# Kernel optimization log

Measured on AMD Instinct MI355X. Metric: run time of the kernel, lower is better.

Reference implementation:

```python
import jax, jax.numpy as jnp
import numpy as np

B, N, K, C = 8, 4096, 32, 64
RADIUS = 0.15
CIN = C + 3  # dp_fj: concat(dp[3], fj[C])


def _ball_query(p, radius, k):
    """p: (B,N,3). Returns neighbor indices (B,N,K): first k points (in index
    order) within radius of each query, padded with the first valid neighbor
    (ballquery semantics; query point itself is always index 0 candidate)."""
    sq = jnp.sum(p * p, axis=-1)                                  # (B,N)
    d2 = sq[:, :, None] + sq[:, None, :] - 2.0 * jnp.einsum('bnd,bmd->bnm', p, p)
    n = p.shape[1]
    within = d2 <= radius * radius
    key = jnp.where(within, jnp.arange(n, dtype=jnp.int32)[None, None, :], n)
    order = jnp.argsort(key, axis=-1)[..., :k]                    # (B,N,K)
    valid = jnp.take_along_axis(key, order, axis=-1) < n
    first = order[..., :1]
    return jnp.where(valid, order, first)


def _conv2d_1x1(x, w, b):
    # x: (B,Cin,N,K), w: (Cout,Cin), b: (Cout,)
    return jnp.einsum('oi,bink->bonk', w, x) + b[None, :, None, None]


def _conv1d_1x1(x, w, b):
    # x: (B,Cin,N)
    return jnp.einsum('oi,bin->bon', w, x) + b[None, :, None]


def setup_inputs() -> dict:
    key = jax.random.key(0)
    ks = jax.random.split(key, 16)
    s = 0.05
    inp = {
        'p': jax.random.uniform(ks[0], (B, N, 3), dtype=jnp.float32),
        'f': jax.random.normal(ks[1], (B, C, N), dtype=jnp.float32),
        # attn_local: convblock2d (CIN -> C), no act
        'w_attn': jax.random.normal(ks[2], (C, CIN), dtype=jnp.float32) * s,
        'b_attn': jnp.zeros((C,), jnp.float32),
        # convs: convblock2d (CIN -> C, relu) then (C -> C, no act)
        'w1': jax.random.normal(ks[3], (C, CIN), dtype=jnp.float32) * s,
        'b1': jnp.zeros((C,), jnp.float32),
        'w2': jax.random.normal(ks[4], (C, C), dtype=jnp.float32) * s,
        'b2': jnp.zeros((C,), jnp.float32),
        # ffn: convblock1d (C -> C*expansion=C, relu) then (C -> C, no act)
        'wf1': jax.random.normal(ks[5], (C, C), dtype=jnp.float32) * s,
        'bf1': jnp.zeros((C,), jnp.float32),
        'wf2': jax.random.normal(ks[6], (C, C), dtype=jnp.float32) * s,
        'bf2': jnp.zeros((C,), jnp.float32),
    }
    return inp


def reference(p, f, w_attn, b_attn, w1, b1, w2, b2, wf1, bf1, wf2, bf2):
    bidx = jnp.arange(B)[:, None, None]
    idx = _ball_query(p, RADIUS, K)                               # (B,N,K) int
    pj = p[bidx, idx]                                             # (B,N,K,3)
    dp = (pj - p[:, :, None, :]).transpose(0, 3, 1, 2)            # (B,3,N,K)
    ft = f.transpose(0, 2, 1)                                     # (B,N,C)
    fj = ft[bidx, idx].transpose(0, 3, 1, 2)                      # (B,C,N,K)

    fj_cat = jnp.concatenate([dp, fj], axis=1)                    # (B,CIN,N,K)

    attn = _conv2d_1x1(fj_cat, w_attn, b_attn)                    # (B,C,N,K)
    x = jax.nn.relu(_conv2d_1x1(fj_cat, w1, b1))
    x = _conv2d_1x1(x, w2, b2)                                    # (B,C,N,K)

    # new_attention, 4D path: softmax over neighbor axis (tau=1), weighted sum
    channel_attn = jax.nn.softmax(attn, axis=-1)
    fout = jnp.sum(channel_attn * x, axis=-1)                     # (B,C,N)

    fout = jax.nn.relu(fout + f)
    identity = fout
    h = jax.nn.relu(_conv1d_1x1(fout, wf1, bf1))
    h = _conv1d_1x1(h, wf2, bf2)
    fout = jax.nn.relu(h + identity)                              # use_res
    return (p, fout)
```

## Files before the change

kernel.cpp:

```cpp
#include <hip/hip_runtime.h>

#define B_ 8
#define N_ 4096
#define K_ 32
#define C_ 64
#define CIN_ 67
#define R2_ 0.0225f

#define SFJ 104
#define SY1 72
#define SFB 72
#define PTS 4
#define ITERS 4

typedef short short8v __attribute__((ext_vector_type(8)));
typedef short short4v __attribute__((ext_vector_type(4)));
typedef float floatx4 __attribute__((ext_vector_type(4)));

__device__ __forceinline__ short f2bf(float x) {
    return (short)__builtin_bit_cast(unsigned short, (__bf16)x);
}

template <int CTRL>
__device__ __forceinline__ float dpp_add(float x) {
    const int m = __builtin_amdgcn_update_dpp(0, __float_as_int(x), CTRL, 0xF, 0xF, false);
    return x + __int_as_float(m);
}
__device__ __forceinline__ float row16_sum(float x) {
    x = dpp_add<0xB1>(x);
    x = dpp_add<0x4E>(x);
    x = dpp_add<0x141>(x);
    x = dpp_add<0x140>(x);
    return x;
}

__global__ __launch_bounds__(256) void prep_kernel(
    const float* __restrict__ p, const float* __restrict__ f,
    unsigned short* __restrict__ ftb, float4* __restrict__ p4,
    float* __restrict__ pout)
{
#pragma clang fp contract(off)
    __shared__ short tile[64 * 72];
    const int t = threadIdx.x;
    const int b = blockIdx.x >> 6;
    const int n0 = (blockIdx.x & 63) * 64;
    const int nn4 = t & 15, ch = t >> 4;
    for (int cc = 0; cc < 4; ++cc) {
        const int c = cc * 16 + ch;
        const float4 v = *(const float4*)&f[((size_t)(b * 64 + c)) * N_ + n0 + nn4 * 4];
        tile[(nn4 * 4 + 0) * 72 + c] = f2bf(v.x);
        tile[(nn4 * 4 + 1) * 72 + c] = f2bf(v.y);
        tile[(nn4 * 4 + 2) * 72 + c] = f2bf(v.z);
        tile[(nn4 * 4 + 3) * 72 + c] = f2bf(v.w);
    }
    if (t < 48) {
        const size_t base = ((size_t)(b * N_ + n0)) * 3;
        ((float4*)(pout + base))[t] = ((const float4*)(p + base))[t];
    }
    if (t < 64) {
        const int n = n0 + t;
        const float x = p[((size_t)(b * N_ + n)) * 3 + 0];
        const float y = p[((size_t)(b * N_ + n)) * 3 + 1];
        const float z = p[((size_t)(b * N_ + n)) * 3 + 2];
        const float sq = (x * x + y * y) + z * z;
        p4[(size_t)b * N_ + n] = make_float4(x, y, z, sq);
    }
    __syncthreads();
    const int nn = t >> 2, cb = (t & 3) * 16;
    uint4* dst = (uint4*)&ftb[((size_t)(b * N_ + n0 + nn)) * 64 + cb];
    const uint4* src = (const uint4*)&tile[nn * 72 + cb];
    dst[0] = src[0];
    dst[1] = src[1];
}

__global__ __launch_bounds__(256) void ball_query_kernel(
    const float4* __restrict__ p4, unsigned short* __restrict__ idx)
{
#pragma clang fp contract(off)
    const int lane = threadIdx.x & 63;
    const int wid = (blockIdx.x * blockDim.x + threadIdx.x) >> 6;
    const int q0 = wid * 4;
    const int b = q0 >> 12;
    const float4* pb = p4 + (size_t)b * N_;

    float4 Q[4];
    #pragma unroll
    for (int q = 0; q < 4; ++q)
        Q[q] = pb[(q0 + q) & (N_ - 1)];
    int count[4] = {0, 0, 0, 0};
    int first[4] = {-1, -1, -1, -1};
    for (int base = 0; base < N_; base += 64) {
        const float4 A = pb[base + lane];
        unsigned long long m[4];
        bool w[4];
        #pragma unroll
        for (int q = 0; q < 4; ++q) {
            const float d2 = (Q[q].w + A.w)
                - 2.0f * ((Q[q].x * A.x + Q[q].y * A.y) + Q[q].z * A.z);
            w[q] = (d2 <= R2_);
            m[q] = __ballot(w[q]);
        }
        const unsigned long long below = (1ull << lane) - 1ull;
        #pragma unroll
        for (int q = 0; q < 4; ++q) {
            if (m[q]) {
                if (first[q] < 0) first[q] = base + __builtin_ctzll(m[q]);
                if (w[q]) {
                    const int pos = count[q] + __popcll(m[q] & below);
                    if (pos < K_)
                        idx[(size_t)(q0 + q) * K_ + pos] = (unsigned short)(base + lane);
                }
                count[q] += __popcll(m[q]);
            }
        }
        if (count[0] >= K_ && count[1] >= K_ && count[2] >= K_ && count[3] >= K_)
            break;
    }
    #pragma unroll
    for (int q = 0; q < 4; ++q)
        for (int pos = count[q] + lane; pos < K_; pos += 64)
            idx[(size_t)(q0 + q) * K_ + pos] = (unsigned short)first[q];
}

__global__ __launch_bounds__(256) void lpa_mfma_kernel(
    const float4* __restrict__ p4, const float* __restrict__ f,
    const unsigned short* __restrict__ ftb,
    const float* __restrict__ w_attn, const float* __restrict__ b_attn,
    const float* __restrict__ w1, const float* __restrict__ b1,
    const float* __restrict__ w2, const float* __restrict__ b2,
    const float* __restrict__ wf1, const float* __restrict__ bf1,
    const float* __restrict__ wf2, const float* __restrict__ bf2,
    const unsigned short* __restrict__ idx, float* __restrict__ out)
{
    __shared__ __align__(16) short s_fj[128 * SFJ];
    __shared__ __align__(16) short s_y1[128 * SY1];
    __shared__ __align__(16) short s_fbuf[2 * 16 * SFB];
    __shared__ float s_vec[PTS * ITERS * 64];
    short* s_vecbf = s_fbuf;
    short* s_hbf   = s_fbuf + 16 * SFB;

    const int t = threadIdx.x;
    const int lane = t & 63;
    const int mb = t >> 6;
    const int l15 = lane & 15;
    const int quad = lane >> 4;

    short8v wa_f[3], w1_f[3], w2_f[2], wf1_f[2], wf2_f[2];
    {
        const int cm = mb * 16 + l15;
        #pragma unroll
        for (int ks = 0; ks < 3; ++ks) {
            short8v a, bq;
            #pragma unroll
            for (int j = 0; j < 8; ++j) {
                const int ip = ks * 32 + quad * 8 + j;
                float va = 0.0f, vb = 0.0f;
                if (ip < 64)      { va = w_attn[cm * CIN_ + ip + 3];  vb = w1[cm * CIN_ + ip + 3]; }
                else if (ip < 67) { va = w_attn[cm * CIN_ + ip - 64]; vb = w1[cm * CIN_ + ip - 64]; }
                a[j] = f2bf(va); bq[j] = f2bf(vb);
            }
            wa_f[ks] = a; w1_f[ks] = bq;
        }
        #pragma unroll
        for (int ks = 0; ks < 2; ++ks) {
            short8v a, bq, cq;
            #pragma unroll
            for (int j = 0; j < 8; ++j) {
                const int kk = ks * 32 + quad * 8 + j;
                a[j]  = f2bf(w2[cm * 64 + kk]);
                bq[j] = f2bf(wf1[cm * 64 + kk]);
                cq[j] = f2bf(wf2[cm * 64 + kk]);
            }
            w2_f[ks] = a; wf1_f[ks] = bq; wf2_f[ks] = cq;
        }
    }

    const int crow = mb * 16 + quad * 4;
    const float4 bav  = *(const float4*)&b_attn[crow];
    const float4 b1v  = *(const float4*)&b1[crow];
    const float4 b2v  = *(const float4*)&b2[crow];
    const float4 bf1v = *(const float4*)&bf1[crow];
    const float4 bf2v = *(const float4*)&bf2[crow];

    for (int e = t; e < 512; e += 256) {
        const int col = e >> 2, c4 = e & 3;
        *(uint4*)&s_fj[col * SFJ + 72 + c4 * 8] = make_uint4(0u, 0u, 0u, 0u);
    }
    for (int e = t; e < 1152; e += 256) ((unsigned*)s_fbuf)[e] = 0u;

    const int pt00 = blockIdx.x * (PTS * ITERS);
    const int bb = pt00 >> 12;
    const float4* pb = p4 + (size_t)bb * N_;

    const int col = t >> 1, h = t & 1;

    {
        const int j = idx[(size_t)pt00 * K_ + col];
        const uint4* src = (const uint4*)&ftb[((size_t)(bb * N_ + j)) * 64 + h * 32];
        uint4* dst = (uint4*)&s_fj[col * SFJ + h * 32];
        dst[0] = src[0]; dst[1] = src[1]; dst[2] = src[2]; dst[3] = src[3];
        if (h) {
            const int n = (pt00 + (col >> 5)) & (N_ - 1);
            const float4 Pj = pb[j];
            const float4 Pn = pb[n];
            short8v dp = {};
            dp[0] = f2bf(Pj.x - Pn.x);
            dp[1] = f2bf(Pj.y - Pn.y);
            dp[2] = f2bf(Pj.z - Pn.z);
            *(short8v*)&s_fj[col * SFJ + 64] = dp;
        }
    }
    __syncthreads();

    for (int itn = 0; itn < ITERS; ++itn) {
        const int pt0 = pt00 + itn * PTS;

        const bool pf = (itn + 1 < ITERS);
        uint4 g0, g1, g2, g3;
        float4 Pjn, Pnn;
        if (pf) {
            const int jn = idx[(size_t)(pt0 + PTS) * K_ + col];
            const uint4* src = (const uint4*)&ftb[((size_t)(bb * N_ + jn)) * 64 + h * 32];
            g0 = src[0]; g1 = src[1]; g2 = src[2]; g3 = src[3];
            Pjn = pb[jn];
            Pnn = pb[(pt0 + PTS + (col >> 5)) & (N_ - 1)];
        }

        floatx4 accA[8];
        #pragma unroll
        for (int nt = 0; nt < 8; ++nt) {
            const short* bp = &s_fj[(nt * 16 + l15) * SFJ + quad * 8];
            const short8v fb0 = *(const short8v*)(bp);
            const short8v fb1 = *(const short8v*)(bp + 32);
            const short8v fb2 = *(const short8v*)(bp + 64);
            floatx4 a = {0.f, 0.f, 0.f, 0.f};
            a = __builtin_amdgcn_mfma_f32_16x16x32_bf16(wa_f[0], fb0, a, 0, 0, 0);
            a = __builtin_amdgcn_mfma_f32_16x16x32_bf16(wa_f[1], fb1, a, 0, 0, 0);
            a = __builtin_amdgcn_mfma_f32_16x16x32_bf16(wa_f[2], fb2, a, 0, 0, 0);
            accA[nt] = a;
            floatx4 y = {0.f, 0.f, 0.f, 0.f};
            y = __builtin_amdgcn_mfma_f32_16x16x32_bf16(w1_f[0], fb0, y, 0, 0, 0);
            y = __builtin_amdgcn_mfma_f32_16x16x32_bf16(w1_f[1], fb1, y, 0, 0, 0);
            y = __builtin_amdgcn_mfma_f32_16x16x32_bf16(w1_f[2], fb2, y, 0, 0, 0);
            short4v yp;
            yp[0] = f2bf(fmaxf(y[0] + b1v.x, 0.f));
            yp[1] = f2bf(fmaxf(y[1] + b1v.y, 0.f));
            yp[2] = f2bf(fmaxf(y[2] + b1v.z, 0.f));
            yp[3] = f2bf(fmaxf(y[3] + b1v.w, 0.f));
            *(short4v*)&s_y1[(nt * 16 + l15) * SY1 + crow] = yp;
        }
        __syncthreads();

        if (pf) {
            uint4* dst = (uint4*)&s_fj[col * SFJ + h * 32];
            dst[0] = g0; dst[1] = g1; dst[2] = g2; dst[3] = g3;
            if (h) {
                short8v dp = {};
                dp[0] = f2bf(Pjn.x - Pnn.x);
                dp[1] = f2bf(Pjn.y - Pnn.y);
                dp[2] = f2bf(Pjn.z - Pnn.z);
                *(short8v*)&s_fj[col * SFJ + 64] = dp;
            }
        }

        const int nb0 = pt0 & (N_ - 1);
        float4 f4r[4];
        #pragma unroll
        for (int r = 0; r < 4; ++r)
            f4r[r] = *(const float4*)&f[((size_t)(bb * 64 + crow + r)) * N_ + nb0];

        #pragma unroll
        for (int pi = 0; pi < PTS; ++pi) {
            floatx4 xx0, xx1;
            {
                const short* bp = &s_y1[((2 * pi) * 16 + l15) * SY1 + quad * 8];
                const short8v yb0 = *(const short8v*)(bp);
                const short8v yb1 = *(const short8v*)(bp + 32);
                floatx4 x = {0.f, 0.f, 0.f, 0.f};
                x = __builtin_amdgcn_mfma_f32_16x16x32_bf16(w2_f[0], yb0, x, 0, 0, 0);
                x = __builtin_amdgcn_mfma_f32_16x16x32_bf16(w2_f[1], yb1, x, 0, 0, 0);
                xx0 = x;
            }
            {
                const short* bp = &s_y1[((2 * pi + 1) * 16 + l15) * SY1 + quad * 8];
                const short8v yb0 = *(const short8v*)(bp);
                const short8v yb1 = *(const short8v*)(bp + 32);
                floatx4 x = {0.f, 0.f, 0.f, 0.f};
                x = __builtin_amdgcn_mfma_f32_16x16x32_bf16(w2_f[0], yb0, x, 0, 0, 0);
                x = __builtin_amdgcn_mfma_f32_16x16x32_bf16(w2_f[1], yb1, x, 0, 0, 0);
                xx1 = x;
            }
            float fo[4];
            #pragma unroll
            for (int r = 0; r < 4; ++r) {
                const float ba = (r == 0) ? bav.x : (r == 1) ? bav.y : (r == 2) ? bav.z : bav.w;
                const float bx = (r == 0) ? b2v.x : (r == 1) ? b2v.y : (r == 2) ? b2v.z : b2v.w;
                const float e0 = __expf(accA[2 * pi][r] + ba);
                const float e1 = __expf(accA[2 * pi + 1][r] + ba);
                const float t01 = e0 + e1;
                const float se = row16_sum(t01);
                const float sw = row16_sum(e0 * xx0[r] + e1 * xx1[r] + t01 * bx);
                const float fres = (pi == 0) ? f4r[r].x : (pi == 1) ? f4r[r].y
                                 : (pi == 2) ? f4r[r].z : f4r[r].w;
                fo[r] = fmaxf(sw * __builtin_amdgcn_rcpf(se) + fres, 0.f);
            }
            if (l15 == 0) {
                const int prow = itn * PTS + pi;
                *(float4*)&s_vec[prow * 64 + crow] = make_float4(fo[0], fo[1], fo[2], fo[3]);
                short4v fb;
                fb[0] = f2bf(fo[0]); fb[1] = f2bf(fo[1]);
                fb[2] = f2bf(fo[2]); fb[3] = f2bf(fo[3]);
                *(short4v*)&s_vecbf[prow * SFB + crow] = fb;
            }
        }
        __syncthreads();
    }

    {
        const short8v vb0 = *(const short8v*)&s_vecbf[l15 * SFB + quad * 8];
        const short8v vb1 = *(const short8v*)&s_vecbf[l15 * SFB + 32 + quad * 8];
        floatx4 d = {0.f, 0.f, 0.f, 0.f};
        d = __builtin_amdgcn_mfma_f32_16x16x32_bf16(wf1_f[0], vb0, d, 0, 0, 0);
        d = __builtin_amdgcn_mfma_f32_16x16x32_bf16(wf1_f[1], vb1, d, 0, 0, 0);
        short4v hb;
        hb[0] = f2bf(fmaxf(d[0] + bf1v.x, 0.f));
        hb[1] = f2bf(fmaxf(d[1] + bf1v.y, 0.f));
        hb[2] = f2bf(fmaxf(d[2] + bf1v.z, 0.f));
        hb[3] = f2bf(fmaxf(d[3] + bf1v.w, 0.f));
        *(short4v*)&s_hbf[l15 * SFB + crow] = hb;
    }
    __syncthreads();

    {
        const short8v hb0 = *(const short8v*)&s_hbf[l15 * SFB + quad * 8];
        const short8v hb1 = *(const short8v*)&s_hbf[l15 * SFB + 32 + quad * 8];
        floatx4 d = {0.f, 0.f, 0.f, 0.f};
        d = __builtin_amdgcn_mfma_f32_16x16x32_bf16(wf2_f[0], hb0, d, 0, 0, 0);
        d = __builtin_amdgcn_mfma_f32_16x16x32_bf16(wf2_f[1], hb1, d, 0, 0, 0);
        const int n = (pt00 + l15) & (N_ - 1);
        out[((size_t)(bb * 64 + crow + 0)) * N_ + n] =
            fmaxf(d[0] + bf2v.x + s_vec[l15 * 64 + crow + 0], 0.f);
        out[((size_t)(bb * 64 + crow + 1)) * N_ + n] =
            fmaxf(d[1] + bf2v.y + s_vec[l15 * 64 + crow + 1], 0.f);
        out[((size_t)(bb * 64 + crow + 2)) * N_ + n] =
            fmaxf(d[2] + bf2v.z + s_vec[l15 * 64 + crow + 2], 0.f);
        out[((size_t)(bb * 64 + crow + 3)) * N_ + n] =
            fmaxf(d[3] + bf2v.w + s_vec[l15 * 64 + crow + 3], 0.f);
    }
}

extern "C" void kernel_launch(void* const* d_in, const int* in_sizes, int n_in,
                              void* d_out, int out_size, void* d_ws, size_t ws_size,
                              hipStream_t stream)
{
    const float* p      = (const float*)d_in[0];
    const float* f      = (const float*)d_in[1];
    const float* w_attn = (const float*)d_in[2];
    const float* b_attn = (const float*)d_in[3];
    const float* w1     = (const float*)d_in[4];
    const float* b1     = (const float*)d_in[5];
    const float* w2     = (const float*)d_in[6];
    const float* b2     = (const float*)d_in[7];
    const float* wf1    = (const float*)d_in[8];
    const float* bf1    = (const float*)d_in[9];
    const float* wf2    = (const float*)d_in[10];
    const float* bf2    = (const float*)d_in[11];
    float* out = (float*)d_out;

    unsigned short* idx = (unsigned short*)d_ws;
    unsigned short* ftb = (unsigned short*)((char*)d_ws + 2u * 1024 * 1024);
    float4* p4          = (float4*)((char*)d_ws + 6u * 1024 * 1024);

    prep_kernel<<<B_ * (N_ / 64), 256, 0, stream>>>(p, f, ftb, p4, out);
    ball_query_kernel<<<(B_ * N_) / 16, 256, 0, stream>>>(p4, idx);
    lpa_mfma_kernel<<<(B_ * N_) / (PTS * ITERS), 256, 0, stream>>>(
        p4, f, ftb, w_attn, b_attn, w1, b1, w2, b2, wf1, bf1, wf2, bf2,
        idx, out + (size_t)B_ * N_ * 3);
}
```

Before: 222.2 us.

## Double-buffer LDS tiles with XOR swizzle and drop a per-iteration barrier

Replaces padded LDS rows with an unpadded 64-column layout using an XOR swizzle to avoid bank conflicts. The dp channels move to a separate small buffer, injected only by quad 0 for the third k-slice. The fj and y1 tiles are double-buffered so one barrier per iteration replaces two. This cuts barrier stalls and LDS footprint, at the cost of extra index math and a more delicate ordering between writing the next buffer and reading the current one.

```diff
diff --git a/kernel.cpp b/kernel.cpp
--- a/kernel.cpp
+++ b/kernel.cpp
@@ -7,9 +7,6 @@
 #define CIN_ 67
 #define R2_ 0.0225f
 
-#define SFJ 104
-#define SY1 72
-#define SFB 72
 #define PTS 4
 #define ITERS 4
 
@@ -132,12 +129,13 @@
     const float* __restrict__ wf2, const float* __restrict__ bf2,
     const unsigned short* __restrict__ idx, float* __restrict__ out)
 {
-    __shared__ __align__(16) short s_fj[128 * SFJ];
-    __shared__ __align__(16) short s_y1[128 * SY1];
-    __shared__ __align__(16) short s_fbuf[2 * 16 * SFB];
-    __shared__ float s_vec[PTS * ITERS * 64];
+    __shared__ __align__(16) short s_fj[2][128 * 64];
+    __shared__ __align__(16) short s_dp[2][128 * 8];
+    __shared__ __align__(16) short s_y1[2][128 * 64];
+    __shared__ __align__(16) short s_fbuf[2 * 16 * 64];
+    __shared__ float s_vec[16 * 64];
     short* s_vecbf = s_fbuf;
-    short* s_hbf   = s_fbuf + 16 * SFB;
+    short* s_hbf   = s_fbuf + 16 * 64;
 
     const int t = threadIdx.x;
     const int lane = t & 63;
@@ -182,23 +180,21 @@
     const float4 bf1v = *(const float4*)&bf1[crow];
     const float4 bf2v = *(const float4*)&bf2[crow];
 
-    for (int e = t; e < 512; e += 256) {
-        const int col = e >> 2, c4 = e & 3;
-        *(uint4*)&s_fj[col * SFJ + 72 + c4 * 8] = make_uint4(0u, 0u, 0u, 0u);
-    }
-    for (int e = t; e < 1152; e += 256) ((unsigned*)s_fbuf)[e] = 0u;
-
     const int pt00 = blockIdx.x * (PTS * ITERS);
     const int bb = pt00 >> 12;
     const float4* pb = p4 + (size_t)bb * N_;
 
     const int col = t >> 1, h = t & 1;
+    const int gsw = (col & 7) << 3;
 
     {
         const int j = idx[(size_t)pt00 * K_ + col];
         const uint4* src = (const uint4*)&ftb[((size_t)(bb * N_ + j)) * 64 + h * 32];
-        uint4* dst = (uint4*)&s_fj[col * SFJ + h * 32];
-        dst[0] = src[0]; dst[1] = src[1]; dst[2] = src[2]; dst[3] = src[3];
+        const int rb = col * 64;
+        *(uint4*)&s_fj[0][rb + ((h * 32 + 0)  ^ gsw)] = src[0];
+        *(uint4*)&s_fj[0][rb + ((h * 32 + 8)  ^ gsw)] = src[1];
+        *(uint4*)&s_fj[0][rb + ((h * 32 + 16) ^ gsw)] = src[2];
+        *(uint4*)&s_fj[0][rb + ((h * 32 + 24) ^ gsw)] = src[3];
         if (h) {
             const int n = (pt00 + (col >> 5)) & (N_ - 1);
             const float4 Pj = pb[j];
@@ -207,13 +203,14 @@
             dp[0] = f2bf(Pj.x - Pn.x);
             dp[1] = f2bf(Pj.y - Pn.y);
             dp[2] = f2bf(Pj.z - Pn.z);
-            *(short8v*)&s_fj[col * SFJ + 64] = dp;
+            *(short8v*)&s_dp[0][col * 8] = dp;
         }
     }
     __syncthreads();
 
     for (int itn = 0; itn < ITERS; ++itn) {
         const int pt0 = pt00 + itn * PTS;
+        const int cur = itn & 1, nxt = cur ^ 1;
 
         const bool pf = (itn + 1 < ITERS);
         uint4 g0, g1, g2, g3;
@@ -229,10 +226,14 @@
         floatx4 accA[8];
         #pragma unroll
         for (int nt = 0; nt < 8; ++nt) {
-            const short* bp = &s_fj[(nt * 16 + l15) * SFJ + quad * 8];
-            const short8v fb0 = *(const short8v*)(bp);
-            const short8v fb1 = *(const short8v*)(bp + 32);
-            const short8v fb2 = *(const short8v*)(bp + 64);
+            const int row = nt * 16 + l15;
+            const int sw = (l15 & 7) << 3;
+            const short* bp = &s_fj[cur][row * 64];
+            const short8v fb0 = *(const short8v*)(bp + ((quad * 8) ^ sw));
+            const short8v fb1 = *(const short8v*)(bp + ((32 + quad * 8) ^ sw));
+            const short8v dpv = *(const short8v*)&s_dp[cur][row * 8];
+            short8v fb2 = {};
+            if (quad == 0) fb2 = dpv;
             floatx4 a = {0.f, 0.f, 0.f, 0.f};
             a = __builtin_amdgcn_mfma_f32_16x16x32_bf16(wa_f[0], fb0, a, 0, 0, 0);
             a = __builtin_amdgcn_mfma_f32_16x16x32_bf16(wa_f[1], fb1, a, 0, 0, 0);
@@ -247,21 +248,24 @@
             yp[1] = f2bf(fmaxf(y[1] + b1v.y, 0.f));
             yp[2] = f2bf(fmaxf(y[2] + b1v.z, 0.f));
             yp[3] = f2bf(fmaxf(y[3] + b1v.w, 0.f));
-            *(short4v*)&s_y1[(nt * 16 + l15) * SY1 + crow] = yp;
-        }
-        __syncthreads();
+            *(short4v*)&s_y1[cur][row * 64 + (crow ^ sw)] = yp;
+        }
 
         if (pf) {
-            uint4* dst = (uint4*)&s_fj[col * SFJ + h * 32];
-            dst[0] = g0; dst[1] = g1; dst[2] = g2; dst[3] = g3;
+            const int rb = col * 64;
+            *(uint4*)&s_fj[nxt][rb + ((h * 32 + 0)  ^ gsw)] = g0;
+            *(uint4*)&s_fj[nxt][rb + ((h * 32 + 8)  ^ gsw)] = g1;
+            *(uint4*)&s_fj[nxt][rb + ((h * 32 + 16) ^ gsw)] = g2;
+            *(uint4*)&s_fj[nxt][rb + ((h * 32 + 24) ^ gsw)] = g3;
             if (h) {
                 short8v dp = {};
                 dp[0] = f2bf(Pjn.x - Pnn.x);
                 dp[1] = f2bf(Pjn.y - Pnn.y);
                 dp[2] = f2bf(Pjn.z - Pnn.z);
-                *(short8v*)&s_fj[col * SFJ + 64] = dp;
-            }
-        }
+                *(short8v*)&s_dp[nxt][col * 8] = dp;
+            }
+        }
+        __syncthreads();
 
         const int nb0 = pt0 & (N_ - 1);
         float4 f4r[4];
@@ -273,18 +277,22 @@
         for (int pi = 0; pi < PTS; ++pi) {
             floatx4 xx0, xx1;
             {
-                const short* bp = &s_y1[((2 * pi) * 16 + l15) * SY1 + quad * 8];
-                const short8v yb0 = *(const short8v*)(bp);
-                const short8v yb1 = *(const short8v*)(bp + 32);
+                const int row = (2 * pi) * 16 + l15;
+                const int sw = (l15 & 7) << 3;
+                const short* bp = &s_y1[cur][row * 64];
+                const short8v yb0 = *(const short8v*)(bp + ((quad * 8) ^ sw));
+                const short8v yb1 = *(const short8v*)(bp + ((32 + quad * 8) ^ sw));
                 floatx4 x = {0.f, 0.f, 0.f, 0.f};
                 x = __builtin_amdgcn_mfma_f32_16x16x32_bf16(w2_f[0], yb0, x, 0, 0, 0);
                 x = __builtin_amdgcn_mfma_f32_16x16x32_bf16(w2_f[1], yb1, x, 0, 0, 0);
                 xx0 = x;
             }
             {
-                const short* bp = &s_y1[((2 * pi + 1) * 16 + l15) * SY1 + quad * 8];
-                const short8v yb0 = *(const short8v*)(bp);
-                const short8v yb1 = *(const short8v*)(bp + 32);
+                const int row = (2 * pi + 1) * 16 + l15;
+                const int sw = (l15 & 7) << 3;
+                const short* bp = &s_y1[cur][row * 64];
+                const short8v yb0 = *(const short8v*)(bp + ((quad * 8) ^ sw));
+                const short8v yb1 = *(const short8v*)(bp + ((32 + quad * 8) ^ sw));
                 floatx4 x = {0.f, 0.f, 0.f, 0.f};
                 x = __builtin_amdgcn_mfma_f32_16x16x32_bf16(w2_f[0], yb0, x, 0, 0, 0);
                 x = __builtin_amdgcn_mfma_f32_16x16x32_bf16(w2_f[1], yb1, x, 0, 0, 0);
@@ -299,10 +307,10 @@
                 const float e1 = __expf(accA[2 * pi + 1][r] + ba);
                 const float t01 = e0 + e1;
                 const float se = row16_sum(t01);
-                const float sw = row16_sum(e0 * xx0[r] + e1 * xx1[r] + t01 * bx);
+                const float sw_ = row16_sum(e0 * xx0[r] + e1 * xx1[r] + t01 * bx);
                 const float fres = (pi == 0) ? f4r[r].x : (pi == 1) ? f4r[r].y
                                  : (pi == 2) ? f4r[r].z : f4r[r].w;
-                fo[r] = fmaxf(sw * __builtin_amdgcn_rcpf(se) + fres, 0.f);
+                fo[r] = fmaxf(sw_ * __builtin_amdgcn_rcpf(se) + fres, 0.f);
             }
             if (l15 == 0) {
                 const int prow = itn * PTS + pi;
@@ -310,15 +318,16 @@
                 short4v fb;
                 fb[0] = f2bf(fo[0]); fb[1] = f2bf(fo[1]);
                 fb[2] = f2bf(fo[2]); fb[3] = f2bf(fo[3]);
-                *(short4v*)&s_vecbf[prow * SFB + crow] = fb;
-            }
-        }
-        __syncthreads();
-    }
+                *(short4v*)&s_vecbf[prow * 64 + (crow ^ ((prow & 7) << 3))] = fb;
+            }
+        }
+    }
+    __syncthreads();
 
     {
-        const short8v vb0 = *(const short8v*)&s_vecbf[l15 * SFB + quad * 8];
-        const short8v vb1 = *(const short8v*)&s_vecbf[l15 * SFB + 32 + quad * 8];
+        const int sw = (l15 & 7) << 3;
+        const short8v vb0 = *(const short8v*)&s_vecbf[l15 * 64 + ((quad * 8) ^ sw)];
+        const short8v vb1 = *(const short8v*)&s_vecbf[l15 * 64 + ((32 + quad * 8) ^ sw)];
         floatx4 d = {0.f, 0.f, 0.f, 0.f};
         d = __builtin_amdgcn_mfma_f32_16x16x32_bf16(wf1_f[0], vb0, d, 0, 0, 0);
         d = __builtin_amdgcn_mfma_f32_16x16x32_bf16(wf1_f[1], vb1, d, 0, 0, 0);
@@ -327,13 +336,14 @@
         hb[1] = f2bf(fmaxf(d[1] + bf1v.y, 0.f));
         hb[2] = f2bf(fmaxf(d[2] + bf1v.z, 0.f));
         hb[3] = f2bf(fmaxf(d[3] + bf1v.w, 0.f));
-        *(short4v*)&s_hbf[l15 * SFB + crow] = hb;
+        *(short4v*)&s_hbf[l15 * 64 + (crow ^ sw)] = hb;
     }
     __syncthreads();
 
     {
-        const short8v hb0 = *(const short8v*)&s_hbf[l15 * SFB + quad * 8];
-        const short8v hb1 = *(const short8v*)&s_hbf[l15 * SFB + 32 + quad * 8];
+        const int sw = (l15 & 7) << 3;
+        const short8v hb0 = *(const short8v*)&s_hbf[l15 * 64 + ((quad * 8) ^ sw)];
+        const short8v hb1 = *(const short8v*)&s_hbf[l15 * 64 + ((32 + quad * 8) ^ sw)];
         floatx4 d = {0.f, 0.f, 0.f, 0.f};
         d = __builtin_amdgcn_mfma_f32_16x16x32_bf16(wf2_f[0], hb0, d, 0, 0, 0);
         d = __builtin_amdgcn_mfma_f32_16x16x32_bf16(wf2_f[1], hb1, d, 0, 0, 0);
```

After: 223.6 us. About the same (+0.6%).
